# Performance work log

Measured on AMD Instinct MI355X. Metric: run time of the kernel, lower is better.

Reference implementation:

```python
import jax, jax.numpy as jnp
import numpy as np

B, S, D = 4, 2048, 128

def _phi(x, W, d):
    # original: phi(x) = (1/sqrt(M)) * exp(-0.5*||x||_2) * exp(W @ x), M = d
    proj = jnp.exp(jnp.einsum('...d,md->...m', x, W))          # [..., d]
    scale = jnp.exp(-0.5 * jnp.linalg.norm(x, axis=-1, keepdims=True))
    return (scale / jnp.sqrt(jnp.asarray(d, x.dtype))) * proj

def setup_inputs() -> dict:
    key = jax.random.key(0)
    k1, k2, k3, k4 = jax.random.split(key, 4)
    # scale 0.1 keeps exp(W @ x) well within fp32 range
    K = jax.random.normal(k1, (B, S, D), dtype=jnp.float32) * 0.1
    Q = jax.random.normal(k2, (B, S, D), dtype=jnp.float32) * 0.1
    V = jax.random.normal(k3, (B, S, D), dtype=jnp.float32) * 0.1
    W_phi = jax.random.normal(k4, (D, D), dtype=jnp.float32)
    sent_embed_slice = jnp.zeros((B, 1), dtype=jnp.float32)
    return {"K": K, "Q": Q, "V": V, "sent_embed_slice": sent_embed_slice,
            "max_seq_length": S, "qkv_size": D, "W_phi": W_phi}

def reference(K, Q, V, sent_embed_slice, max_seq_length, qkv_size, W_phi):
    d = qkv_size
    phiK = _phi(K, W_phi, d)   # [B, S, d]
    phiQ = _phi(Q, W_phi, d)   # [B, S, d]
    Bn = K.shape[0]

    def step(carry, inp):
        Mst, Nst = carry                       # [B, d, d], [B, d]
        pk, v, pq = inp                        # each [B, d]
        Mst = Mst + pk[:, :, None] * v[:, None, :]   # cumulative outer product
        Nst = Nst + pk                               # cumulative feature sum
        num = jnp.einsum('bd,bde->be', pq, Mst)      # phi(q) @ M
        r = jnp.einsum('bd,bd->b', pq, Nst)          # phi(q) . N
        out = num / (r + jnp.sign(r) * 1e-6)[:, None]
        return (Mst, Nst), out

    init = (jnp.zeros((Bn, d, d), K.dtype), jnp.zeros((Bn, d), K.dtype))
    xs = (jnp.swapaxes(phiK, 0, 1), jnp.swapaxes(V, 0, 1), jnp.swapaxes(phiQ, 0, 1))
    _, outs = jax.lax.scan(step, init, xs)    # outs: [S, B, d]
    return jnp.swapaxes(outs, 0, 1)           # [B, S, d]
```

## Files before the change

kernel.cpp:

```cpp
#include <hip/hip_runtime.h>

typedef float v4 __attribute__((ext_vector_type(4)));
typedef short s8v __attribute__((ext_vector_type(8)));
typedef float f4v __attribute__((ext_vector_type(4)));
typedef unsigned short u16;
typedef u16 us2 __attribute__((ext_vector_type(2)));
typedef u16 us4 __attribute__((ext_vector_type(4)));
typedef u16 us8 __attribute__((ext_vector_type(8)));

#define OFF_PHIKB 0
#define OFF_PHIQB 524288
#define OFF_KVTB  1048576
#define OFF_N32   2097152

__device__ inline u16 f2bf(float f) {
  union { float f; unsigned u; } v; v.f = f;
  unsigned r = v.u + 0x7fffu + ((v.u >> 16) & 1u);
  return (u16)(r >> 16);
}
__device__ inline float bf2f(u16 h) {
  union { unsigned u; float f; } v; v.u = ((unsigned)h) << 16; return v.f;
}

__global__ __launch_bounds__(512) void phikv_kernel(
    const float* __restrict__ K, const float* __restrict__ Q,
    const float* __restrict__ V, const float* __restrict__ W,
    u16* __restrict__ phiKb, u16* __restrict__ phiQb,
    u16* __restrict__ KVTb, float* __restrict__ N32) {
  __shared__ __align__(16) u16 smem[27136];
  __shared__ float srowsq[64];
  __shared__ float scl[64];
  u16* Xb = smem;
  u16* Wb = smem + 8704;
  u16* Pb = smem;
  u16* KdT = smem + 8704;
  u16* Vt = smem + 17920;

  const int tid = threadIdx.x;
  const bool isK = (blockIdx.y == 0);
  const float* X = isK ? K : Q;
  u16* outPhi = isK ? phiKb : phiQb;
  const int row0 = blockIdx.x * 64;
  const int wv = tid >> 6;
  const int lane = tid & 63;
  const int q = lane >> 4;
  const int ln = lane & 15;

  v4 vpa[2], vpb[2];
  if (isK) {
#pragma unroll
    for (int k = 0; k < 2; k++) {
      int j = tid + k * 512;
      int s0 = (j & 31) * 2;
      int e4 = (j >> 5) * 4;
      vpa[k] = *(const v4*)&V[(size_t)(row0 + s0) * 128 + e4];
      vpb[k] = *(const v4*)&V[(size_t)(row0 + s0 + 1) * 128 + e4];
    }
  }

#pragma unroll
  for (int k = 0; k < 4; k++) {
    int j = tid + k * 512;
    int r = j >> 5;
    int c4 = (j & 31) * 4;
    v4 x = *(const v4*)&X[(size_t)(row0 + r) * 128 + c4];
    us4 xb;
    float p = 0.f;
#pragma unroll
    for (int i = 0; i < 4; i++) { xb[i] = f2bf(x[i]); p += x[i] * x[i]; }
    *(us4*)&Xb[r * 136 + c4] = xb;
    p += __shfl_down(p, 16, 32);
    p += __shfl_down(p, 8, 32);
    p += __shfl_down(p, 4, 32);
    p += __shfl_down(p, 2, 32);
    p += __shfl_down(p, 1, 32);
    if ((tid & 31) == 0) srowsq[r] = p;
  }
#pragma unroll
  for (int k = 0; k < 8; k++) {
    int j = tid + k * 512;
    int r = j >> 5;
    int c4 = (j & 31) * 4;
    v4 w = *(const v4*)&W[(size_t)r * 128 + c4];
    us4 wb;
#pragma unroll
    for (int i = 0; i < 4; i++) wb[i] = f2bf(w[i]);
    *(us4*)&Wb[r * 136 + c4] = wb;
  }
  __syncthreads();
  if (tid < 64)
    scl[tid] = 0.08838834764831845f * __expf(-0.5f * sqrtf(srowsq[tid]));

  const int tr = wv >> 1;
  const int cb = (wv & 1) * 4;
  f4v acc[4];
#pragma unroll
  for (int i = 0; i < 4; i++) acc[i] = (f4v){0.f, 0.f, 0.f, 0.f};
#pragma unroll
  for (int ks = 0; ks < 4; ks++) {
    s8v a = *(const s8v*)&Xb[(tr * 16 + ln) * 136 + ks * 32 + q * 8];
#pragma unroll
    for (int i = 0; i < 4; i++) {
      s8v bb = *(const s8v*)&Wb[((cb + i) * 16 + ln) * 136 + ks * 32 + q * 8];
      acc[i] = __builtin_amdgcn_mfma_f32_16x16x32_bf16(a, bb, acc[i], 0, 0, 0);
    }
  }
  __syncthreads();

#pragma unroll
  for (int i = 0; i < 4; i++) {
    const int ct = cb + i;
    us4 col;
#pragma unroll
    for (int r = 0; r < 4; r++) {
      int row = tr * 16 + q * 4 + r;
      u16 hv = f2bf(scl[row] * __expf(acc[i][r]));
      Pb[row * 136 + ct * 16 + ln] = hv;
      col[r] = hv;
    }
    if (isK) *(us4*)&KdT[(ct * 16 + ln) * 72 + tr * 16 + q * 4] = col;
  }
  if (isK) {
#pragma unroll
    for (int k = 0; k < 2; k++) {
      int j = tid + k * 512;
      int s0 = (j & 31) * 2;
      int e4 = (j >> 5) * 4;
#pragma unroll
      for (int i = 0; i < 4; i++) {
        us2 w2 = {f2bf(vpa[k][i]), f2bf(vpb[k][i])};
        *(us2*)&Vt[(e4 + i) * 72 + s0] = w2;
      }
    }
  }
  __syncthreads();

#pragma unroll
  for (int k = 0; k < 2; k++) {
    int j = tid + k * 512;
    int r = j >> 4;
    int d8 = (j & 15) * 8;
    *(us8*)&outPhi[(size_t)(row0 + r) * 128 + d8] = *(const us8*)&Pb[r * 136 + d8];
  }
  if (!isK) return;

  const int b = row0 >> 11;
  const int c = (row0 >> 6) & 31;

  if (tid < 128) {
    float ns = 0.f;
#pragma unroll
    for (int s = 0; s < 64; s++) ns += bf2f(KdT[tid * 72 + s]);
    N32[(size_t)(b * 32 + c) * 128 + tid] = ns;
  }

  {
    const int et = wv;
    s8v a0 = *(const s8v*)&Vt[(et * 16 + ln) * 72 + q * 8];
    s8v a1 = *(const s8v*)&Vt[(et * 16 + ln) * 72 + 32 + q * 8];
    f4v ac[8];
#pragma unroll
    for (int dt = 0; dt < 8; dt++) ac[dt] = (f4v){0.f, 0.f, 0.f, 0.f};
#pragma unroll
    for (int dt = 0; dt < 8; dt++) {
      s8v b0 = *(const s8v*)&KdT[(dt * 16 + ln) * 72 + q * 8];
      ac[dt] = __builtin_amdgcn_mfma_f32_16x16x32_bf16(a0, b0, ac[dt], 0, 0, 0);
      s8v b1 = *(const s8v*)&KdT[(dt * 16 + ln) * 72 + 32 + q * 8];
      ac[dt] = __builtin_amdgcn_mfma_f32_16x16x32_bf16(a1, b1, ac[dt], 0, 0, 0);
    }
#pragma unroll
    for (int dt = 0; dt < 8; dt++)
#pragma unroll
      for (int r = 0; r < 4; r++) {
        int e = et * 16 + q * 4 + r;
        int d = dt * 16 + ln;
        KVTb[((size_t)(b * 128 + e) * 32 + c) * 128 + d] = f2bf(ac[dt][r]);
      }
  }
}

__global__ __launch_bounds__(256) void out_kernel(
    const u16* __restrict__ phiKb, const u16* __restrict__ phiQb,
    const float* __restrict__ V, const u16* __restrict__ KVTb,
    const float* __restrict__ N32, float* __restrict__ out) {
  __shared__ __align__(16) u16 Qs[64 * 136];
  __shared__ __align__(16) u16 Ks[64 * 136];
  __shared__ __align__(16) u16 Ms[32 * 136];
  __shared__ __align__(16) u16 Vt[32 * 72];
  __shared__ __align__(16) u16 Ps[64 * 72];
  __shared__ float Ns[128];
  __shared__ float rs[64];

  const int tid = threadIdx.x;
  const int id = blockIdx.x;
  const int c = id >> 4;
  const int g = id & 15;
  const int b = g >> 2;
  const int h = g & 3;
  const int srow0 = b * 2048 + c * 64;
  const int ecol0 = h * 32;
  const int wv = tid >> 6;
  const int lane = tid & 63;
  const int q = lane >> 4;
  const int ln = lane & 15;

  const int vs0 = (tid & 31) * 2;
  const int ve4 = (tid >> 5) * 4;
  v4 va = *(const v4*)&V[(size_t)(srow0 + vs0) * 128 + ecol0 + ve4];
  v4 vb = *(const v4*)&V[(size_t)(srow0 + vs0 + 1) * 128 + ecol0 + ve4];

#pragma unroll
  for (int k = 0; k < 4; k++) {
    int j = tid + k * 256;
    int t = j >> 4;
    int d8 = (j & 15) * 8;
    *(us8*)&Qs[t * 136 + d8] = *(const us8*)&phiQb[(size_t)(srow0 + t) * 128 + d8];
    *(us8*)&Ks[t * 136 + d8] = *(const us8*)&phiKb[(size_t)(srow0 + t) * 128 + d8];
  }

  {
    const int se = tid >> 4;
    const int sd8 = (tid & 15) * 8;
    const u16* src0 =
        &KVTb[((size_t)(b * 128 + ecol0 + se) * 32) * 128 + sd8];
    const u16* src1 =
        &KVTb[((size_t)(b * 128 + ecol0 + 16 + se) * 32) * 128 + sd8];
    float m0[8], m1[8];
#pragma unroll
    for (int i = 0; i < 8; i++) { m0[i] = 0.f; m1[i] = 0.f; }
    for (int base = 0; base < c; base += 8) {
      us8 t0[8], t1[8];
#pragma unroll
      for (int u = 0; u < 8; u++) {
        if (base + u < c) {
          t0[u] = *(const us8*)&src0[(base + u) * 128];
          t1[u] = *(const us8*)&src1[(base + u) * 128];
        }
      }
#pragma unroll
      for (int u = 0; u < 8; u++) {
        if (base + u < c) {
#pragma unroll
          for (int i = 0; i < 8; i++) {
            m0[i] += bf2f(t0[u][i]);
            m1[i] += bf2f(t1[u][i]);
          }
        }
      }
    }
    us8 w0, w1;
#pragma unroll
    for (int i = 0; i < 8; i++) { w0[i] = f2bf(m0[i]); w1[i] = f2bf(m1[i]); }
    *(us8*)&Ms[se * 136 + sd8] = w0;
    *(us8*)&Ms[(16 + se) * 136 + sd8] = w1;
  }
  if (tid < 128) {
    float na = 0.f;
    for (int base = 0; base < c; base += 8) {
      float t[8];
#pragma unroll
      for (int u = 0; u < 8; u++)
        t[u] = (base + u < c) ? N32[(size_t)(b * 32 + base + u) * 128 + tid]
                              : 0.f;
#pragma unroll
      for (int u = 0; u < 8; u++) na += t[u];
    }
    Ns[tid] = na;
  }
#pragma unroll
  for (int i = 0; i < 4; i++) {
    us2 w2 = {f2bf(va[i]), f2bf(vb[i])};
    *(us2*)&Vt[(ve4 + i) * 72 + vs0] = w2;
  }
  __syncthreads();

  {
    const int tr = wv;
    for (int tc = 0; tc < 4; tc++) {
      f4v acc = {0.f, 0.f, 0.f, 0.f};
      if (tc <= tr) {
#pragma unroll
        for (int ks = 0; ks < 4; ks++) {
          s8v a = *(const s8v*)&Qs[(tr * 16 + ln) * 136 + ks * 32 + q * 8];
          s8v bb = *(const s8v*)&Ks[(tc * 16 + ln) * 136 + ks * 32 + q * 8];
          acc = __builtin_amdgcn_mfma_f32_16x16x32_bf16(a, bb, acc, 0, 0, 0);
        }
      }
      const int s_g = tc * 16 + ln;
#pragma unroll
      for (int r = 0; r < 4; r++) {
        int t_g = tr * 16 + q * 4 + r;
        Ps[t_g * 72 + s_g] = f2bf(s_g <= t_g ? acc[r] : 0.f);
      }
    }
  }
  __syncthreads();

  {
    const int t = tid >> 2;
    const int p4 = tid & 3;
    float rsl = 0.f;
#pragma unroll
    for (int s = p4; s < 64; s += 4) rsl += bf2f(Ps[t * 72 + s]);
#pragma unroll
    for (int d = p4; d < 128; d += 4) rsl += bf2f(Qs[t * 136 + d]) * Ns[d];
    rsl += __shfl_down(rsl, 2, 4);
    rsl += __shfl_down(rsl, 1, 4);
    if (p4 == 0) rs[t] = rsl;
  }

  const int et = wv & 1;
  f4v acc2[2];
#pragma unroll
  for (int i = 0; i < 2; i++) acc2[i] = (f4v){0.f, 0.f, 0.f, 0.f};
#pragma unroll
  for (int i = 0; i < 2; i++) {
    const int tr2 = (wv >> 1) + 2 * i;
#pragma unroll
    for (int ks2 = 0; ks2 < 2; ks2++) {
      s8v a_p = *(const s8v*)&Ps[(tr2 * 16 + ln) * 72 + ks2 * 32 + q * 8];
      s8v b_v = *(const s8v*)&Vt[(et * 16 + ln) * 72 + ks2 * 32 + q * 8];
      acc2[i] = __builtin_amdgcn_mfma_f32_16x16x32_bf16(a_p, b_v, acc2[i], 0, 0, 0);
    }
#pragma unroll
    for (int ks = 0; ks < 4; ks++) {
      s8v a_q = *(const s8v*)&Qs[(tr2 * 16 + ln) * 136 + ks * 32 + q * 8];
      s8v b_m = *(const s8v*)&Ms[(et * 16 + ln) * 136 + ks * 32 + q * 8];
      acc2[i] = __builtin_amdgcn_mfma_f32_16x16x32_bf16(a_q, b_m, acc2[i], 0, 0, 0);
    }
  }
  __syncthreads();

#pragma unroll
  for (int i = 0; i < 2; i++) {
    const int tr2 = (wv >> 1) + 2 * i;
#pragma unroll
    for (int r = 0; r < 4; r++) {
      int t_g = tr2 * 16 + q * 4 + r;
      float rv = rs[t_g];
      float den = rv + (rv > 0.f ? 1e-6f : (rv < 0.f ? -1e-6f : 0.f));
      out[(size_t)(srow0 + t_g) * 128 + ecol0 + et * 16 + ln] =
          acc2[i][r] / den;
    }
  }
}

extern "C" void kernel_launch(void* const* d_in, const int* in_sizes, int n_in,
                              void* d_out, int out_size, void* d_ws,
                              size_t ws_size, hipStream_t stream) {
  (void)in_sizes; (void)n_in; (void)out_size; (void)ws_size;
  const float* K = (const float*)d_in[0];
  const float* Q = (const float*)d_in[1];
  const float* V = (const float*)d_in[2];
  const float* W = (const float*)d_in[6];
  float* out = (float*)d_out;
  float* ws = (float*)d_ws;

  u16* phiKb = (u16*)(ws + OFF_PHIKB);
  u16* phiQb = (u16*)(ws + OFF_PHIQB);
  u16* KVTb = (u16*)(ws + OFF_KVTB);
  float* N32 = ws + OFF_N32;

  phikv_kernel<<<dim3(128, 2), 512, 0, stream>>>(K, Q, V, W, phiKb, phiQb,
                                                 KVTb, N32);
  out_kernel<<<512, 256, 0, stream>>>(phiKb, phiQb, V, KVTb, N32, out);
}
```

Baseline: 97.28 us.

## Add separate exclusive prefix-scan kernel for chunk KV and N states

Adds a scan kernel that computes exclusive prefix sums of the per-chunk KV outer products and feature sums once. The output kernel then loads its prefix state directly instead of each block re-summing up to 31 earlier chunks, which removed quadratic redundant reads of the KVTb buffer. In exchange there is an extra kernel launch, a new small serial kernel with only 132 blocks of 64 threads, and an extra global round trip for the prefix buffers. It also vectorises the N32 column-sum loads in phikv_kernel.

```diff
diff --git a/kernel.cpp b/kernel.cpp
--- a/kernel.cpp
+++ b/kernel.cpp
@@ -12,6 +12,8 @@
 #define OFF_PHIQB 524288
 #define OFF_KVTB  1048576
 #define OFF_N32   2097152
+#define OFF_MPRE  2113536
+#define OFF_NPRE  3162112
 
 __device__ inline u16 f2bf(float f) {
   union { float f; unsigned u; } v; v.f = f;
@@ -150,7 +152,11 @@
   if (tid < 128) {
     float ns = 0.f;
 #pragma unroll
-    for (int s = 0; s < 64; s++) ns += bf2f(KdT[tid * 72 + s]);
+    for (int s8 = 0; s8 < 64; s8 += 8) {
+      us8 v = *(const us8*)&KdT[tid * 72 + s8];
+#pragma unroll
+      for (int i = 0; i < 8; i++) ns += bf2f(v[i]);
+    }
     N32[(size_t)(b * 32 + c) * 128 + tid] = ns;
   }
 
@@ -179,10 +185,52 @@
   }
 }
 
+__global__ __launch_bounds__(64) void scan_kernel(
+    const u16* __restrict__ KVTb, const float* __restrict__ N32,
+    u16* __restrict__ Mpre, float* __restrict__ Npre) {
+  const int id = blockIdx.x;
+  const int tid = threadIdx.x;
+  if (id < 128) {
+    const int b = id >> 5;
+    const int e = (id & 31) * 4 + (tid >> 4);
+    const int d8 = (tid & 15) * 8;
+    const u16* src = &KVTb[((size_t)(b * 128 + e) * 32) * 128 + d8];
+    u16* dst = &Mpre[((size_t)b * 32 * 128 + e) * 128 + d8];
+    float acc[8];
+#pragma unroll
+    for (int i = 0; i < 8; i++) acc[i] = 0.f;
+    for (int base = 0; base < 32; base += 8) {
+      us8 t[8];
+#pragma unroll
+      for (int u = 0; u < 8; u++) t[u] = *(const us8*)&src[(base + u) * 128];
+#pragma unroll
+      for (int u = 0; u < 8; u++) {
+        us8 w;
+#pragma unroll
+        for (int i = 0; i < 8; i++) w[i] = f2bf(acc[i]);
+        *(us8*)&dst[(size_t)(base + u) * 16384] = w;
+#pragma unroll
+        for (int i = 0; i < 8; i++) acc[i] += bf2f(t[u][i]);
+      }
+    }
+  } else {
+    const int b = id - 128;
+    const float* src = &N32[(size_t)b * 32 * 128 + tid];
+    float* dst = &Npre[(size_t)b * 32 * 128 + tid];
+    float a0 = 0.f, a1 = 0.f;
+    for (int cc = 0; cc < 32; cc++) {
+      dst[cc * 128] = a0;
+      dst[cc * 128 + 64] = a1;
+      a0 += src[cc * 128];
+      a1 += src[cc * 128 + 64];
+    }
+  }
+}
+
 __global__ __launch_bounds__(256) void out_kernel(
     const u16* __restrict__ phiKb, const u16* __restrict__ phiQb,
-    const float* __restrict__ V, const u16* __restrict__ KVTb,
-    const float* __restrict__ N32, float* __restrict__ out) {
+    const float* __restrict__ V, const u16* __restrict__ Mpre,
+    const float* __restrict__ Npre, float* __restrict__ out) {
   __shared__ __align__(16) u16 Qs[64 * 136];
   __shared__ __align__(16) u16 Ks[64 * 136];
   __shared__ __align__(16) u16 Ms[32 * 136];
@@ -221,52 +269,11 @@
   {
     const int se = tid >> 4;
     const int sd8 = (tid & 15) * 8;
-    const u16* src0 =
-        &KVTb[((size_t)(b * 128 + ecol0 + se) * 32) * 128 + sd8];
-    const u16* src1 =
-        &KVTb[((size_t)(b * 128 + ecol0 + 16 + se) * 32) * 128 + sd8];
-    float m0[8], m1[8];
-#pragma unroll
-    for (int i = 0; i < 8; i++) { m0[i] = 0.f; m1[i] = 0.f; }
-    for (int base = 0; base < c; base += 8) {
-      us8 t0[8], t1[8];
-#pragma unroll
-      for (int u = 0; u < 8; u++) {
-        if (base + u < c) {
-          t0[u] = *(const us8*)&src0[(base + u) * 128];
-          t1[u] = *(const us8*)&src1[(base + u) * 128];
-        }
-      }
-#pragma unroll
-      for (int u = 0; u < 8; u++) {
-        if (base + u < c) {
-#pragma unroll
-          for (int i = 0; i < 8; i++) {
-            m0[i] += bf2f(t0[u][i]);
-            m1[i] += bf2f(t1[u][i]);
-          }
-        }
-      }
-    }
-    us8 w0, w1;
-#pragma unroll
-    for (int i = 0; i < 8; i++) { w0[i] = f2bf(m0[i]); w1[i] = f2bf(m1[i]); }
-    *(us8*)&Ms[se * 136 + sd8] = w0;
-    *(us8*)&Ms[(16 + se) * 136 + sd8] = w1;
-  }
-  if (tid < 128) {
-    float na = 0.f;
-    for (int base = 0; base < c; base += 8) {
-      float t[8];
-#pragma unroll
-      for (int u = 0; u < 8; u++)
-        t[u] = (base + u < c) ? N32[(size_t)(b * 32 + base + u) * 128 + tid]
-                              : 0.f;
-#pragma unroll
-      for (int u = 0; u < 8; u++) na += t[u];
-    }
-    Ns[tid] = na;
-  }
+    const u16* mp = &Mpre[((size_t)(b * 32 + c) * 128 + ecol0) * 128 + sd8];
+    *(us8*)&Ms[se * 136 + sd8] = *(const us8*)&mp[se * 128];
+    *(us8*)&Ms[(16 + se) * 136 + sd8] = *(const us8*)&mp[(16 + se) * 128];
+  }
+  if (tid < 128) Ns[tid] = Npre[(size_t)(b * 32 + c) * 128 + tid];
 #pragma unroll
   for (int i = 0; i < 4; i++) {
     us2 w2 = {f2bf(va[i]), f2bf(vb[i])};
@@ -360,8 +367,11 @@
   u16* phiQb = (u16*)(ws + OFF_PHIQB);
   u16* KVTb = (u16*)(ws + OFF_KVTB);
   float* N32 = ws + OFF_N32;
+  u16* Mpre = (u16*)(ws + OFF_MPRE);
+  float* Npre = ws + OFF_NPRE;
 
   phikv_kernel<<<dim3(128, 2), 512, 0, stream>>>(K, Q, V, W, phiKb, phiQb,
                                                  KVTb, N32);
-  out_kernel<<<512, 256, 0, stream>>>(phiKb, phiQb, V, KVTb, N32, out);
-}
+  scan_kernel<<<132, 64, 0, stream>>>(KVTb, N32, Mpre, Npre);
+  out_kernel<<<512, 256, 0, stream>>>(phiKb, phiQb, V, Mpre, Npre, out);
+}
```

Measured after the change: 93.00 us. 1.05x faster.
